# Optimization experiments

Hardware: AMD Instinct MI355X
Metric: run time of the kernel (lower is better)

The kernel has to match this reference:

```python
import jax, jax.numpy as jnp
import numpy as np

H = 1024      # lstm_hidden_size
LABELS = 122  # slot label size


def setup_inputs() -> dict:
    key = jax.random.key(0)
    ks = jax.random.split(key, 8)
    s_in = 1.0 / np.sqrt(5 * H)
    s_h = 1.0 / np.sqrt(H)
    return {
        "x": jax.random.normal(ks[0], (1, 512, 2 * H), jnp.float32),
        "hi": jax.random.normal(ks[1], (1, 512, 2 * H), jnp.float32),
        # LSTM params (PyTorch layout: gates ordered i, f, g, o)
        "W_ih": jax.random.uniform(ks[2], (4 * H, 5 * H), jnp.float32, -s_in, s_in),
        "W_hh": jax.random.uniform(ks[3], (4 * H, H), jnp.float32, -s_h, s_h),
        "b_ih": jax.random.uniform(ks[4], (4 * H,), jnp.float32, -s_h, s_h),
        "b_hh": jax.random.uniform(ks[5], (4 * H,), jnp.float32, -s_h, s_h),
        "W_fc": jax.random.uniform(ks[6], (LABELS, H), jnp.float32, -s_h, s_h),
        "b_fc": jax.random.uniform(ks[7], (LABELS,), jnp.float32, -s_h, s_h),
    }


def _decode(x, hi, W_ih, W_hh, b_ih, b_hh, W_fc, b_fc):
    # x, hi: [1, L, 2H] -> per-step encoder features [L, 4H] (batch fixed at 1)
    feats = jnp.concatenate([x, hi], axis=-1)[0]
    bias = b_ih + b_hh

    def step(carry, f_t):
        h, c, prev_out = carry
        z = jnp.concatenate([f_t, prev_out])              # [5H]: cat(x_t, hi_t, out_{t-1})
        gates = W_ih @ z + W_hh @ h + bias                # [4H]
        i, f, g, o = jnp.split(gates, 4)
        c_new = jax.nn.sigmoid(f) * c + jax.nn.sigmoid(i) * jnp.tanh(g)
        h_new = jax.nn.sigmoid(o) * jnp.tanh(c_new)
        return (h_new, c_new, h_new), h_new

    zero = jnp.zeros((H,), x.dtype)
    _, outs = jax.lax.scan(step, (zero, zero, zero), feats)  # outs: [L, H]
    res = outs @ W_fc.T + b_fc                               # [L, LABELS]
    return res[None]                                         # [1, L, LABELS]


def reference(x, hi, W_ih, W_hh, b_ih, b_hh, W_fc, b_fc):
    return _decode(x, hi, W_ih, W_hh, b_ih, b_hh, W_fc, b_fc)
```

## Files before the change

kernel.cpp:

```cpp
#include <hip/hip_runtime.h>
#include <hip/hip_fp16.h>
#include <math.h>

#define HD    1024
#define SEQL  512
#define NLAB  122
#define NWG   128
#define TPW   512
#define JPW   8

#define OFF_MSG   ((size_t)0)
#define OFF_HALL  ((size_t)16384)
#define OFF_GATES ((size_t)2113536)
#define OFF_WR    ((size_t)10502144)
#define OFF_W1H   ((size_t)27279360)
#define OFF_FH    ((size_t)60833792)
#define WS_NEED   ((size_t)65028096)
#define REP_MAX   8
#define OFF_MSG8  WS_NEED
#define WS_NEED8  (WS_NEED + (size_t)2 * REP_MAX * HD * 8)

typedef unsigned long long u64;
typedef _Float16 v8h __attribute__((ext_vector_type(8)));
typedef float v4f __attribute__((ext_vector_type(4)));
typedef float v2f __attribute__((ext_vector_type(2)));
typedef unsigned int v4u __attribute__((ext_vector_type(4)));

__global__ __launch_bounds__(256) void prep_wr(const float* __restrict__ W_ih,
                                               const float* __restrict__ W_hh,
                                               float* __restrict__ W_r2) {
    int o = blockIdx.x * 256 + threadIdx.x;
    int g   = o >> 13;
    int i   = (o >> 9) & 15;
    int t   = o & 511;
    int row = t & 31;
    int kq  = t >> 5;
    int gate = row >> 3;
    int jj   = row & 7;
    int R = (gate << 10) + (g << 3) + jj;
    int k = (kq << 6) + (i << 2);
    float4 wa = *(const float4*)(W_ih + (size_t)R * 5120 + 4096 + k);
    float4 wb = *(const float4*)(W_hh + (size_t)R * 1024 + k);
    float4 out;
    out.x = wa.x + wb.x; out.y = wa.y + wb.y; out.z = wa.z + wb.z; out.w = wa.w + wb.w;
    *(float4*)(W_r2 + (size_t)o * 4) = out;
}

static __device__ __forceinline__ uint4 pack8(float4 f0, float4 f1) {
    __half2 p0 = __floats2half2_rn(f0.x, f0.y);
    __half2 p1 = __floats2half2_rn(f0.z, f0.w);
    __half2 p2 = __floats2half2_rn(f1.x, f1.y);
    __half2 p3 = __floats2half2_rn(f1.z, f1.w);
    uint4 o;
    o.x = *(unsigned*)&p0; o.y = *(unsigned*)&p1;
    o.z = *(unsigned*)&p2; o.w = *(unsigned*)&p3;
    return o;
}

__global__ __launch_bounds__(256) void prep_fh(const float* __restrict__ x,
                                               const float* __restrict__ hi,
                                               uint4* __restrict__ F_h) {
    int o = blockIdx.x * 256 + threadIdx.x;
    int t = o >> 9;
    int u = o & 511;
    const float* src = (u < 256) ? (x  + (size_t)t * 2048 + u * 8)
                                 : (hi + (size_t)t * 2048 + (u - 256) * 8);
    F_h[o] = pack8(*(const float4*)src, *(const float4*)(src + 4));
}

__global__ __launch_bounds__(256) void prep_w1h(const float* __restrict__ W_ih,
                                                uint4* __restrict__ W1h) {
    int o = blockIdx.x * 256 + threadIdx.x;
    int r = o >> 9;
    int u = o & 511;
    const float* src = W_ih + (size_t)r * 5120 + u * 8;
    W1h[o] = pack8(*(const float4*)src, *(const float4*)(src + 4));
}

__global__ __launch_bounds__(256) void gates_mfma(const uint4* __restrict__ F_u4,
                                                  const uint4* __restrict__ W_u4,
                                                  const float* __restrict__ b_ih,
                                                  const float* __restrict__ b_hh,
                                                  float* __restrict__ gates_x) {
    __shared__ uint4 AsB[1024];
    const _Float16* Ash = (const _Float16*)AsB;
    const _Float16* Bsh = Ash + 4096;
    const int tid  = threadIdx.x;
    const int wv   = tid >> 6;
    const int lane = tid & 63;
    const int wr   = wv & 1;
    const int wc   = wv >> 1;
    const int n0 = blockIdx.x * 128;
    const int t0 = blockIdx.y * 128;

    const int u0 = tid * 2, u1 = tid * 2 + 1;
    const uint4* aSrc0 = F_u4 + (size_t)(t0 + (u0 >> 2)) * 512 + (u0 & 3);
    const uint4* aSrc1 = F_u4 + (size_t)(t0 + (u1 >> 2)) * 512 + (u1 & 3);
    const uint4* bSrc0 = W_u4 + (size_t)(n0 + (u0 >> 2)) * 512 + (u0 & 3);
    const uint4* bSrc1 = W_u4 + (size_t)(n0 + (u1 >> 2)) * 512 + (u1 & 3);

    v4f acc[4][4];
    #pragma unroll
    for (int mi = 0; mi < 4; ++mi)
        #pragma unroll
        for (int ni = 0; ni < 4; ++ni)
            acc[mi][ni] = (v4f){0.f, 0.f, 0.f, 0.f};

    const int aoff = (wr * 64 + (lane & 15)) * 32 + (lane >> 4) * 8;
    const int boff = (wc * 64 + (lane & 15)) * 32 + (lane >> 4) * 8;

    for (int it = 0; it < 128; ++it) {
        uint4 a0 = aSrc0[it * 4], a1 = aSrc1[it * 4];
        uint4 b0 = bSrc0[it * 4], b1 = bSrc1[it * 4];
        __syncthreads();
        AsB[u0]       = a0; AsB[u1]       = a1;
        AsB[512 + u0] = b0; AsB[512 + u1] = b1;
        __syncthreads();
        v8h a8[4], b8[4];
        #pragma unroll
        for (int mi = 0; mi < 4; ++mi)
            a8[mi] = *(const v8h*)(Ash + aoff + mi * 16 * 32);
        #pragma unroll
        for (int ni = 0; ni < 4; ++ni)
            b8[ni] = *(const v8h*)(Bsh + boff + ni * 16 * 32);
        #pragma unroll
        for (int mi = 0; mi < 4; ++mi)
            #pragma unroll
            for (int ni = 0; ni < 4; ++ni)
                acc[mi][ni] = __builtin_amdgcn_mfma_f32_16x16x32_f16(
                                  a8[mi], b8[ni], acc[mi][ni], 0, 0, 0);
    }

    #pragma unroll
    for (int ni = 0; ni < 4; ++ni) {
        int r = n0 + wc * 64 + ni * 16 + (lane & 15);
        int sidx = ((r & 1023) >> 3) * 32 + (r >> 10) * 8 + (r & 7);
        float bias = b_ih[r] + b_hh[r];
        #pragma unroll
        for (int mi = 0; mi < 4; ++mi) {
            int tb = t0 + wr * 64 + mi * 16 + ((lane >> 4) << 2);
            #pragma unroll
            for (int reg = 0; reg < 4; ++reg)
                gates_x[(size_t)(tb + reg) * 4096 + sidx] = acc[mi][ni][reg] + bias;
        }
    }
}

__global__ __launch_bounds__(256) void gates_gemm_f32(const float* __restrict__ x,
                                                      const float* __restrict__ hi,
                                                      const float* __restrict__ W_ih,
                                                      const float* __restrict__ b_ih,
                                                      const float* __restrict__ b_hh,
                                                      float* __restrict__ gates_x) {
    __shared__ float As[16][68];
    __shared__ float Bs[16][68];
    const int tid = threadIdx.x;
    const int r0 = blockIdx.x * 64;
    const int t0 = blockIdx.y * 64;
    const int tx = tid & 15, ty = tid >> 4;
    const int l   = tid & 63;
    const int kq4 = tid >> 6;

    float acc[4][4] = {};
    for (int kb = 0; kb < 4096; kb += 16) {
        int k = kb + kq4 * 4;
        const float* asrc = (k < 2048) ? (x  + (size_t)(t0 + l) * 2048 + k)
                                       : (hi + (size_t)(t0 + l) * 2048 + (k - 2048));
        float4 a4 = *(const float4*)asrc;
        float4 b4 = *(const float4*)(W_ih + (size_t)(r0 + l) * 5120 + k);
        __syncthreads();
        As[kq4 * 4 + 0][l] = a4.x; As[kq4 * 4 + 1][l] = a4.y;
        As[kq4 * 4 + 2][l] = a4.z; As[kq4 * 4 + 3][l] = a4.w;
        Bs[kq4 * 4 + 0][l] = b4.x; Bs[kq4 * 4 + 1][l] = b4.y;
        Bs[kq4 * 4 + 2][l] = b4.z; Bs[kq4 * 4 + 3][l] = b4.w;
        __syncthreads();
        #pragma unroll
        for (int kk = 0; kk < 16; ++kk) {
            float4 av = *(const float4*)&As[kk][ty * 4];
            float4 bv = *(const float4*)&Bs[kk][tx * 4];
            float a_[4] = {av.x, av.y, av.z, av.w};
            float b_[4] = {bv.x, bv.y, bv.z, bv.w};
            #pragma unroll
            for (int i = 0; i < 4; ++i)
                #pragma unroll
                for (int j = 0; j < 4; ++j)
                    acc[i][j] += a_[i] * b_[j];
        }
    }
    int r = r0 + tx * 4;
    float bias[4];
    #pragma unroll
    for (int j = 0; j < 4; ++j) bias[j] = b_ih[r + j] + b_hh[r + j];
    int gate = r >> 10;
    int g    = (r & 1023) >> 3;
    int jj   = r & 7;
    int sidx = g * 32 + gate * 8 + jj;
    #pragma unroll
    for (int i = 0; i < 4; ++i) {
        float4 o;
        o.x = acc[i][0] + bias[0]; o.y = acc[i][1] + bias[1];
        o.z = acc[i][2] + bias[2]; o.w = acc[i][3] + bias[3];
        *(float4*)(gates_x + (size_t)(t0 + ty * 4 + i) * 4096 + sidx) = o;
    }
}

__global__ __launch_bounds__(512, 1) void lstm_rec(const float* __restrict__ gates_x,
                                                   const float* __restrict__ W_r2,
                                                   float* __restrict__ h_all,
                                                   u64* h_msg, int rep) {
    const int g   = blockIdx.x;
    const int tid = threadIdx.x;
    const int row = tid & 31;
    const int kq  = tid >> 5;
    const int cp  = g & (rep - 1);
    __shared__ float4 W_lds[16][TPW];
    __shared__ float4 h_s4[256];
    __shared__ float  partial[8][36];
    float* h_sf = (float*)h_s4;

    {
        const float4* Wp = (const float4*)W_r2 + (size_t)g * 8192;
        #pragma unroll
        for (int i = 0; i < 16; ++i)
            W_lds[i][tid] = Wp[i * TPW + tid];
    }
    __syncthreads();

    float c = 0.f;
    int budget = 4000000;

    for (int s = 0; s < SEQL; ++s) {
        float gx = 0.f;
        if (tid < 32)
            gx = gates_x[(size_t)s * 4096 + g * 32 + tid];

        asm volatile("" ::: "memory");
        float4 w[16];
        #pragma unroll
        for (int i = 0; i < 16; ++i)
            w[i] = W_lds[i][tid];
        asm volatile("" ::: "memory");

        {
            const u64 addr = (u64)(h_msg +
                                   ((size_t)((s & 1) * rep + cp)) * HD + tid * 2);
            const unsigned want = (unsigned)s;
            v4u ra;
            for (;;) {
                asm volatile(
                    "global_load_dwordx4 %0, %1, off sc1\n\t"
                    "s_waitcnt vmcnt(0)"
                    : "=&v"(ra)
                    : "v"(addr)
                    : "memory");
                if (ra.y == want && ra.w == want) break;
                if (--budget < 0) break;
            }
            ((v2f*)h_sf)[tid] = (v2f){__uint_as_float(ra.x), __uint_as_float(ra.z)};
        }
        asm volatile("" ::: "memory");

        float a0 = 0.f, a1 = 0.f, a2 = 0.f, a3 = 0.f;
        #pragma unroll
        for (int i = 0; i < 16; ++i) {
            float4 h4 = h_s4[kq * 16 + i];
            a0 += w[i].x * h4.x;
            a1 += w[i].y * h4.y;
            a2 += w[i].z * h4.z;
            a3 += w[i].w * h4.w;
        }
        float p = (a0 + a1) + (a2 + a3);
        p += __shfl_xor(p, 32, 64);
        if ((tid & 32) == 0)
            partial[tid >> 6][row] = p;
        __syncthreads();

        if (tid < 32) {
            float sum = gx;
            #pragma unroll
            for (int q = 0; q < 8; ++q) sum += partial[q][tid];
            bool isg = ((tid >> 3) == 2);
            float e   = __expf(isg ? -2.f * sum : -sum);
            float act = isg ? (2.f / (1.f + e) - 1.f) : (1.f / (1.f + e));
            int jj = tid & 7;
            float sf = __shfl(act,  8 + jj, 64);
            float tg = __shfl(act, 16 + jj, 64);
            float so = __shfl(act, 24 + jj, 64);
            if (tid < 8) {
                float si = act;
                c = sf * c + si * tg;
                float th = 2.f / (1.f + __expf(-2.f * c)) - 1.f;
                float h = so * th;
                int j = g * JPW + tid;
                h_all[(size_t)s * HD + j] = h;
                u64 m = ((u64)(unsigned)(s + 1) << 32)
                      | (u64)__float_as_uint(h);
                u64* dst = h_msg + (size_t)(((s + 1) & 1) * rep) * HD + j;
                for (int r = 0; r < rep; ++r)
                    __hip_atomic_store(dst + (size_t)r * HD, m,
                                       __ATOMIC_RELAXED, __HIP_MEMORY_SCOPE_AGENT);
            }
        }
    }
}

__global__ __launch_bounds__(128) void fc_out(const float* __restrict__ h_all,
                                              const float* __restrict__ W_fc,
                                              const float* __restrict__ b_fc,
                                              float* __restrict__ out) {
    const int t0 = blockIdx.x * 4;
    const int tid = threadIdx.x;
    __shared__ float4 h_s[1024];
    const float4* hsrc = (const float4*)(h_all + (size_t)t0 * HD);
    #pragma unroll
    for (int i = 0; i < 8; ++i)
        h_s[tid + i * 128] = hsrc[tid + i * 128];
    __syncthreads();
    if (tid < NLAB) {
        float b = b_fc[tid];
        float acc0 = b, acc1 = b, acc2 = b, acc3 = b;
        const float4* wp = (const float4*)(W_fc + (size_t)tid * HD);
        #pragma unroll 4
        for (int k4 = 0; k4 < 256; ++k4) {
            float4 w = wp[k4];
            float4 h0 = h_s[k4];
            float4 h1 = h_s[256 + k4];
            float4 h2 = h_s[512 + k4];
            float4 h3 = h_s[768 + k4];
            acc0 += w.x*h0.x + w.y*h0.y + w.z*h0.z + w.w*h0.w;
            acc1 += w.x*h1.x + w.y*h1.y + w.z*h1.z + w.w*h1.w;
            acc2 += w.x*h2.x + w.y*h2.y + w.z*h2.z + w.w*h2.w;
            acc3 += w.x*h3.x + w.y*h3.y + w.z*h3.z + w.w*h3.w;
        }
        out[(size_t)(t0 + 0) * NLAB + tid] = acc0;
        out[(size_t)(t0 + 1) * NLAB + tid] = acc1;
        out[(size_t)(t0 + 2) * NLAB + tid] = acc2;
        out[(size_t)(t0 + 3) * NLAB + tid] = acc3;
    }
}

extern "C" void kernel_launch(void* const* d_in, const int* in_sizes, int n_in,
                              void* d_out, int out_size, void* d_ws, size_t ws_size,
                              hipStream_t stream) {
    const float* x    = (const float*)d_in[0];
    const float* hi   = (const float*)d_in[1];
    const float* W_ih = (const float*)d_in[2];
    const float* W_hh = (const float*)d_in[3];
    const float* b_ih = (const float*)d_in[4];
    const float* b_hh = (const float*)d_in[5];
    const float* W_fc = (const float*)d_in[6];
    const float* b_fc = (const float*)d_in[7];
    float* out = (float*)d_out;

    char* ws = (char*)d_ws;
    float* h_all   = (float*)(ws + OFF_HALL);
    float* gates_x = (float*)(ws + OFF_GATES);
    float* W_r2    = (float*)(ws + OFF_WR);
    uint4* W1h     = (uint4*)(ws + OFF_W1H);
    uint4* F_h     = (uint4*)(ws + OFF_FH);

    u64* h_msg;
    int  rep;
    if (ws_size >= WS_NEED8) {
        h_msg = (u64*)(ws + OFF_MSG8);
        rep   = REP_MAX;
        hipMemsetAsync(h_msg, 0, (size_t)2 * REP_MAX * HD * 8, stream);
    } else {
        h_msg = (u64*)(ws + OFF_MSG);
        rep   = 1;
        hipMemsetAsync(h_msg, 0, 16384, stream);
    }

    prep_wr<<<4096, 256, 0, stream>>>(W_ih, W_hh, W_r2);

    if (ws_size >= WS_NEED) {
        prep_fh<<<1024, 256, 0, stream>>>(x, hi, F_h);
        prep_w1h<<<8192, 256, 0, stream>>>(W_ih, W1h);
        dim3 gg(32, 4);
        gates_mfma<<<gg, 256, 0, stream>>>(F_h, W1h, b_ih, b_hh, gates_x);
    } else {
        dim3 gg(64, 8);
        gates_gemm_f32<<<gg, 256, 0, stream>>>(x, hi, W_ih, b_ih, b_hh, gates_x);
    }

    lstm_rec<<<NWG, TPW, 0, stream>>>(gates_x, W_r2, h_all, h_msg, rep);

    fc_out<<<SEQL / 4, 128, 0, stream>>>(h_all, W_fc, b_fc, out);
}
```

Measured before the change: 1.243 ms.

## Fuse prep kernels and memset, merge FC into recurrent kernel, batch gate loads

Merges the three prep kernels and the message-buffer memset into one launch. The final FC projection moves into the persistent recurrent kernel, which waits on a release-flagged final step before running it. Input-gate values are now staged into LDS in chunks of 128 steps instead of one global load per step. The per-step poll issues two loads per iteration and drops the replicated message copies. The aim is to cut launch overhead and per-step latency on the serial critical path, at the cost of more LDS use and a single uncontended message copy that every workgroup polls.

```diff
diff --git a/kernel.cpp b/kernel.cpp
--- a/kernel.cpp
+++ b/kernel.cpp
@@ -16,35 +16,12 @@
 #define OFF_W1H   ((size_t)27279360)
 #define OFF_FH    ((size_t)60833792)
 #define WS_NEED   ((size_t)65028096)
-#define REP_MAX   8
-#define OFF_MSG8  WS_NEED
-#define WS_NEED8  (WS_NEED + (size_t)2 * REP_MAX * HD * 8)
 
 typedef unsigned long long u64;
 typedef _Float16 v8h __attribute__((ext_vector_type(8)));
 typedef float v4f __attribute__((ext_vector_type(4)));
 typedef float v2f __attribute__((ext_vector_type(2)));
 typedef unsigned int v4u __attribute__((ext_vector_type(4)));
-
-__global__ __launch_bounds__(256) void prep_wr(const float* __restrict__ W_ih,
-                                               const float* __restrict__ W_hh,
-                                               float* __restrict__ W_r2) {
-    int o = blockIdx.x * 256 + threadIdx.x;
-    int g   = o >> 13;
-    int i   = (o >> 9) & 15;
-    int t   = o & 511;
-    int row = t & 31;
-    int kq  = t >> 5;
-    int gate = row >> 3;
-    int jj   = row & 7;
-    int R = (gate << 10) + (g << 3) + jj;
-    int k = (kq << 6) + (i << 2);
-    float4 wa = *(const float4*)(W_ih + (size_t)R * 5120 + 4096 + k);
-    float4 wb = *(const float4*)(W_hh + (size_t)R * 1024 + k);
-    float4 out;
-    out.x = wa.x + wb.x; out.y = wa.y + wb.y; out.z = wa.z + wb.z; out.w = wa.w + wb.w;
-    *(float4*)(W_r2 + (size_t)o * 4) = out;
-}
 
 static __device__ __forceinline__ uint4 pack8(float4 f0, float4 f1) {
     __half2 p0 = __floats2half2_rn(f0.x, f0.y);
@@ -57,24 +34,51 @@
     return o;
 }
 
-__global__ __launch_bounds__(256) void prep_fh(const float* __restrict__ x,
-                                               const float* __restrict__ hi,
-                                               uint4* __restrict__ F_h) {
-    int o = blockIdx.x * 256 + threadIdx.x;
-    int t = o >> 9;
-    int u = o & 511;
-    const float* src = (u < 256) ? (x  + (size_t)t * 2048 + u * 8)
-                                 : (hi + (size_t)t * 2048 + (u - 256) * 8);
-    F_h[o] = pack8(*(const float4*)src, *(const float4*)(src + 4));
-}
-
-__global__ __launch_bounds__(256) void prep_w1h(const float* __restrict__ W_ih,
-                                                uint4* __restrict__ W1h) {
-    int o = blockIdx.x * 256 + threadIdx.x;
-    int r = o >> 9;
-    int u = o & 511;
-    const float* src = W_ih + (size_t)r * 5120 + u * 8;
-    W1h[o] = pack8(*(const float4*)src, *(const float4*)(src + 4));
+__global__ __launch_bounds__(256) void prep_all(const float* __restrict__ x,
+                                                const float* __restrict__ hi,
+                                                const float* __restrict__ W_ih,
+                                                const float* __restrict__ W_hh,
+                                                float* __restrict__ W_r2,
+                                                uint4* __restrict__ F_h,
+                                                uint4* __restrict__ W1h,
+                                                u64* __restrict__ h_msg) {
+    int b = blockIdx.x;
+    int tid = threadIdx.x;
+    if (b < 4096) {
+        int o = b * 256 + tid;
+        int g   = o >> 13;
+        int i   = (o >> 9) & 15;
+        int t   = o & 511;
+        int row = t & 31;
+        int kq  = t >> 5;
+        int gate = row >> 3;
+        int jj   = row & 7;
+        int R = (gate << 10) + (g << 3) + jj;
+        int k = (kq << 6) + (i << 2);
+        float4 wa = *(const float4*)(W_ih + (size_t)R * 5120 + 4096 + k);
+        float4 wb = *(const float4*)(W_hh + (size_t)R * 1024 + k);
+        float4 out;
+        out.x = wa.x + wb.x; out.y = wa.y + wb.y;
+        out.z = wa.z + wb.z; out.w = wa.w + wb.w;
+        *(float4*)(W_r2 + (size_t)o * 4) = out;
+    } else if (b == 4096) {
+        #pragma unroll
+        for (int i = 0; i < 8; ++i)
+            h_msg[tid * 8 + i] = 0ull;
+    } else if (b < 5121) {
+        int o = (b - 4097) * 256 + tid;
+        int t = o >> 9;
+        int u = o & 511;
+        const float* src = (u < 256) ? (x  + (size_t)t * 2048 + u * 8)
+                                     : (hi + (size_t)t * 2048 + (u - 256) * 8);
+        F_h[o] = pack8(*(const float4*)src, *(const float4*)(src + 4));
+    } else {
+        int o = (b - 5121) * 256 + tid;
+        int r = o >> 9;
+        int u = o & 511;
+        const float* src = W_ih + (size_t)r * 5120 + u * 8;
+        W1h[o] = pack8(*(const float4*)src, *(const float4*)(src + 4));
+    }
 }
 
 __global__ __launch_bounds__(256) void gates_mfma(const uint4* __restrict__ F_u4,
@@ -204,18 +208,21 @@
     }
 }
 
-__global__ __launch_bounds__(512, 1) void lstm_rec(const float* __restrict__ gates_x,
-                                                   const float* __restrict__ W_r2,
-                                                   float* __restrict__ h_all,
-                                                   u64* h_msg, int rep) {
+__global__ __launch_bounds__(512, 1) void lstm_fc(const float* __restrict__ gates_x,
+                                                  const float* __restrict__ W_r2,
+                                                  float* __restrict__ h_all,
+                                                  u64* h_msg,
+                                                  const float* __restrict__ W_fc,
+                                                  const float* __restrict__ b_fc,
+                                                  float* __restrict__ out) {
     const int g   = blockIdx.x;
     const int tid = threadIdx.x;
     const int row = tid & 31;
     const int kq  = tid >> 5;
-    const int cp  = g & (rep - 1);
     __shared__ float4 W_lds[16][TPW];
     __shared__ float4 h_s4[256];
     __shared__ float  partial[8][36];
+    __shared__ float  gxs[4096];
     float* h_sf = (float*)h_s4;
 
     {
@@ -230,9 +237,20 @@
     int budget = 4000000;
 
     for (int s = 0; s < SEQL; ++s) {
+        if ((s & 127) == 0) {
+            float4* gxs4 = (float4*)gxs;
+            #pragma unroll
+            for (int k = 0; k < 2; ++k) {
+                int o4 = tid + k * 512;
+                int t  = o4 >> 3, c4 = o4 & 7;
+                gxs4[o4] = *(const float4*)(gates_x + (size_t)(s + t) * 4096
+                                            + g * 32 + c4 * 4);
+            }
+            __syncthreads();
+        }
+
         float gx = 0.f;
-        if (tid < 32)
-            gx = gates_x[(size_t)s * 4096 + g * 32 + tid];
+        if (tid < 32) gx = gxs[(s & 127) * 32 + tid];
 
         asm volatile("" ::: "memory");
         float4 w[16];
@@ -242,19 +260,20 @@
         asm volatile("" ::: "memory");
 
         {
-            const u64 addr = (u64)(h_msg +
-                                   ((size_t)((s & 1) * rep + cp)) * HD + tid * 2);
+            const u64 addr = (u64)(h_msg + (size_t)(s & 1) * HD + tid * 2);
             const unsigned want = (unsigned)s;
-            v4u ra;
+            v4u ra, rb;
             for (;;) {
                 asm volatile(
-                    "global_load_dwordx4 %0, %1, off sc1\n\t"
+                    "global_load_dwordx4 %0, %2, off sc1\n\t"
+                    "global_load_dwordx4 %1, %2, off sc1\n\t"
                     "s_waitcnt vmcnt(0)"
-                    : "=&v"(ra)
+                    : "=&v"(ra), "=&v"(rb)
                     : "v"(addr)
                     : "memory");
                 if (ra.y == want && ra.w == want) break;
-                if (--budget < 0) break;
+                if (rb.y == want && rb.w == want) { ra = rb; break; }
+                if (--budget < 0) { ra = rb; break; }
             }
             ((v2f*)h_sf)[tid] = (v2f){__uint_as_float(ra.x), __uint_as_float(ra.z)};
         }
@@ -292,30 +311,54 @@
                 float th = 2.f / (1.f + __expf(-2.f * c)) - 1.f;
                 float h = so * th;
                 int j = g * JPW + tid;
-                h_all[(size_t)s * HD + j] = h;
+                __hip_atomic_store(h_all + (size_t)s * HD + j, h,
+                                   __ATOMIC_RELAXED, __HIP_MEMORY_SCOPE_AGENT);
                 u64 m = ((u64)(unsigned)(s + 1) << 32)
                       | (u64)__float_as_uint(h);
-                u64* dst = h_msg + (size_t)(((s + 1) & 1) * rep) * HD + j;
-                for (int r = 0; r < rep; ++r)
-                    __hip_atomic_store(dst + (size_t)r * HD, m,
-                                       __ATOMIC_RELAXED, __HIP_MEMORY_SCOPE_AGENT);
+                u64* dst = h_msg + (size_t)((s + 1) & 1) * HD + j;
+                if (s + 1 == SEQL)
+                    __hip_atomic_store(dst, m, __ATOMIC_RELEASE,
+                                       __HIP_MEMORY_SCOPE_AGENT);
+                else
+                    __hip_atomic_store(dst, m, __ATOMIC_RELAXED,
+                                       __HIP_MEMORY_SCOPE_AGENT);
             }
         }
     }
-}
-
-__global__ __launch_bounds__(128) void fc_out(const float* __restrict__ h_all,
-                                              const float* __restrict__ W_fc,
-                                              const float* __restrict__ b_fc,
-                                              float* __restrict__ out) {
-    const int t0 = blockIdx.x * 4;
-    const int tid = threadIdx.x;
-    __shared__ float4 h_s[1024];
-    const float4* hsrc = (const float4*)(h_all + (size_t)t0 * HD);
+
+    {
+        const u64 addr = (u64)(h_msg + tid * 2);
+        const unsigned want = (unsigned)SEQL;
+        v4u ra;
+        for (;;) {
+            asm volatile(
+                "global_load_dwordx4 %0, %1, off sc1\n\t"
+                "s_waitcnt vmcnt(0)"
+                : "=&v"(ra) : "v"(addr) : "memory");
+            if (ra.y == want && ra.w == want) break;
+            if (--budget < 0) break;
+        }
+    }
+    __syncthreads();
+
+    const int t0 = g * 4;
+    float4* hst = (float4*)gxs;
     #pragma unroll
-    for (int i = 0; i < 8; ++i)
-        h_s[tid + i * 128] = hsrc[tid + i * 128];
+    for (int k = 0; k < 2; ++k) {
+        int o4 = tid + k * 512;
+        int tt = o4 >> 8;
+        int idx = o4 & 255;
+        const u64 ha = (u64)(h_all + (size_t)(t0 + tt) * HD + idx * 4);
+        v4u hv;
+        asm volatile(
+            "global_load_dwordx4 %0, %1, off sc1\n\t"
+            "s_waitcnt vmcnt(0)"
+            : "=&v"(hv) : "v"(ha) : "memory");
+        hst[o4] = (float4){__uint_as_float(hv.x), __uint_as_float(hv.y),
+                           __uint_as_float(hv.z), __uint_as_float(hv.w)};
+    }
     __syncthreads();
+
     if (tid < NLAB) {
         float b = b_fc[tid];
         float acc0 = b, acc1 = b, acc2 = b, acc3 = b;
@@ -323,10 +366,10 @@
         #pragma unroll 4
         for (int k4 = 0; k4 < 256; ++k4) {
             float4 w = wp[k4];
-            float4 h0 = h_s[k4];
-            float4 h1 = h_s[256 + k4];
-            float4 h2 = h_s[512 + k4];
-            float4 h3 = h_s[768 + k4];
+            float4 h0 = hst[k4];
+            float4 h1 = hst[256 + k4];
+            float4 h2 = hst[512 + k4];
+            float4 h3 = hst[768 + k4];
             acc0 += w.x*h0.x + w.y*h0.y + w.z*h0.z + w.w*h0.w;
             acc1 += w.x*h1.x + w.y*h1.y + w.z*h1.z + w.w*h1.w;
             acc2 += w.x*h2.x + w.y*h2.y + w.z*h2.z + w.w*h2.w;
@@ -353,37 +396,22 @@
     float* out = (float*)d_out;
 
     char* ws = (char*)d_ws;
+    u64*   h_msg   = (u64*)(ws + OFF_MSG);
     float* h_all   = (float*)(ws + OFF_HALL);
     float* gates_x = (float*)(ws + OFF_GATES);
     float* W_r2    = (float*)(ws + OFF_WR);
     uint4* W1h     = (uint4*)(ws + OFF_W1H);
     uint4* F_h     = (uint4*)(ws + OFF_FH);
 
-    u64* h_msg;
-    int  rep;
-    if (ws_size >= WS_NEED8) {
-        h_msg = (u64*)(ws + OFF_MSG8);
-        rep   = REP_MAX;
-        hipMemsetAsync(h_msg, 0, (size_t)2 * REP_MAX * HD * 8, stream);
-    } else {
-        h_msg = (u64*)(ws + OFF_MSG);
-        rep   = 1;
-        hipMemsetAsync(h_msg, 0, 16384, stream);
-    }
-
-    prep_wr<<<4096, 256, 0, stream>>>(W_ih, W_hh, W_r2);
-
     if (ws_size >= WS_NEED) {
-        prep_fh<<<1024, 256, 0, stream>>>(x, hi, F_h);
-        prep_w1h<<<8192, 256, 0, stream>>>(W_ih, W1h);
+        prep_all<<<13313, 256, 0, stream>>>(x, hi, W_ih, W_hh, W_r2, F_h, W1h, h_msg);
         dim3 gg(32, 4);
         gates_mfma<<<gg, 256, 0, stream>>>(F_h, W1h, b_ih, b_hh, gates_x);
     } else {
+        prep_all<<<4097, 256, 0, stream>>>(x, hi, W_ih, W_hh, W_r2, F_h, W1h, h_msg);
         dim3 gg(64, 8);
         gates_gemm_f32<<<gg, 256, 0, stream>>>(x, hi, W_ih, b_ih, b_hh, gates_x);
     }
 
-    lstm_rec<<<NWG, TPW, 0, stream>>>(gates_x, W_r2, h_all, h_msg, rep);
-
-    fc_out<<<SEQL / 4, 128, 0, stream>>>(h_all, W_fc, b_fc, out);
-}
+    lstm_fc<<<NWG, TPW, 0, stream>>>(gates_x, W_r2, h_all, h_msg, W_fc, b_fc, out);
+}
```

New measurement: 1.246 ms. Within noise of the previous version (+0.3%).
